# Kernel tuning notes

Hardware: AMD Instinct MI355X
Metric: run time of the kernel (lower is better)

## Reference

```python
import jax, jax.numpy as jnp
import numpy as np

N_NODES = 50000
N_EDGES = 800000
N_GRAPHS = 64
D = 90


def _kaiming_uniform(key, shape, fan_in):
    # kaiming_uniform_ with nonlinearity='relu': gain=sqrt(2), bound=gain*sqrt(3/fan_in)
    bound = np.sqrt(2.0) * np.sqrt(3.0 / fan_in)
    return jax.random.uniform(key, shape, jnp.float32, -bound, bound)


def setup_inputs() -> dict:
    key = jax.random.key(0)
    ks = jax.random.split(key, 16)
    x = jax.random.normal(ks[0], (N_NODES, D), jnp.float32)
    edge_index = jax.random.randint(ks[1], (2, N_EDGES), 0, N_NODES, jnp.int64)
    batch = jnp.sort(jax.random.randint(ks[2], (N_NODES,), 0, N_GRAPHS, jnp.int64))
    inp = {"x": x, "edge_index": edge_index, "batch": batch}
    # SAGEConv params: lin_l (neighbor path, with bias), lin_r (root path, no bias)
    for i, (kl, kr) in enumerate([(ks[3], ks[4]), (ks[5], ks[6]), (ks[7], ks[8])], start=1):
        inp[f"W{i}l"] = _kaiming_uniform(kl, (D, D), D)
        inp[f"b{i}"] = jnp.zeros((D,), jnp.float32)
        inp[f"W{i}r"] = _kaiming_uniform(kr, (D, D), D)
    inp["Wf1"] = _kaiming_uniform(ks[9], (32, D), D)
    inp["bf1"] = jnp.zeros((32,), jnp.float32)
    inp["Wf2"] = _kaiming_uniform(ks[10], (1, 32), 32)
    inp["bf2"] = jnp.zeros((1,), jnp.float32)
    return inp


def _sage_conv(x, src, dst, Wl, bl, Wr):
    # mean-aggregate neighbor messages x[src] at dst, then lin_l(agg) + lin_r(x)
    msg = x[src]                                           # [E, D] gather
    agg = jax.ops.segment_sum(msg, dst, num_segments=N_NODES)  # [N, D] scatter-add
    deg = jax.ops.segment_sum(jnp.ones((src.shape[0],), x.dtype), dst,
                              num_segments=N_NODES)
    agg = agg / jnp.maximum(deg, 1.0)[:, None]
    return agg @ Wl.T + bl + x @ Wr.T


def reference(x, edge_index, batch, W1l, b1, W1r, W2l, b2, W2r, W3l, b3, W3r,
              Wf1, bf1, Wf2, bf2):
    src, dst = edge_index[0], edge_index[1]
    h = jax.nn.relu(_sage_conv(x, src, dst, W1l, b1, W1r))
    h = jax.nn.relu(_sage_conv(h, src, dst, W2l, b2, W2r))
    h = jax.nn.relu(_sage_conv(h, src, dst, W3l, b3, W3r))
    # global_mean_pool over graph ids
    sums = jax.ops.segment_sum(h, batch, num_segments=N_GRAPHS)      # [G, D]
    cnts = jax.ops.segment_sum(jnp.ones((h.shape[0],), h.dtype), batch,
                               num_segments=N_GRAPHS)
    pooled = sums / jnp.maximum(cnts, 1.0)[:, None]
    h4 = jax.nn.relu(pooled @ Wf1.T + bf1)
    return h4 @ Wf2.T + bf2  # [G, 1]
```

## Files before the change

kernel.cpp:

```cpp
#include <hip/hip_runtime.h>
#include <hip/hip_bf16.h>

#define N_NODES 50000
#define N_PAD   50048
#define N_EDGES 800000
#define N_GRAPHS 64
#define D 90
#define HS  96
#define HSD 48
#define H8D 32
#define SC  192

#define NBUCKETS 196
#define BSHIFT 8
#define BIN_EPB 4096

typedef __attribute__((ext_vector_type(8))) short bf16x8;
typedef __attribute__((ext_vector_type(4))) float f32x4;
typedef __attribute__((ext_vector_type(2))) float f32x2;
typedef __attribute__((ext_vector_type(4))) unsigned int u32x4;

__device__ __forceinline__ float bflo(unsigned int v) { return __uint_as_float(v << 16); }
__device__ __forceinline__ float bfhi(unsigned int v) { return __uint_as_float(v & 0xffff0000u); }
__device__ __forceinline__ unsigned short bf16bits(float f) {
    __hip_bfloat16 b = __float2bfloat16(f);
    return *(unsigned short*)&b;
}
__device__ __forceinline__ unsigned int pack2bf(float lo, float hi) {
    return (unsigned int)bf16bits(lo) | ((unsigned int)bf16bits(hi) << 16);
}
__device__ __forceinline__ unsigned char f32_to_fp8(float v) {
    int pk = __builtin_amdgcn_cvt_pk_fp8_f32(v, v, 0, false);
    return (unsigned char)(pk & 0xff);
}
__device__ __forceinline__ void acc_fp8_dword(float* a, unsigned int u) {
    f32x2 lo = __builtin_amdgcn_cvt_pk_f32_fp8((int)u, false);
    f32x2 hi = __builtin_amdgcn_cvt_pk_f32_fp8((int)u, true);
    a[0] += lo.x; a[1] += lo.y; a[2] += hi.x; a[3] += hi.y;
}

__global__ void k_prep(const float* __restrict__ x, __hip_bfloat16* __restrict__ h0,
                       unsigned char* __restrict__ h8a, unsigned char* __restrict__ h8b,
                       const float* __restrict__ w1l, const float* __restrict__ w1r,
                       const float* __restrict__ w2l, const float* __restrict__ w2r,
                       const float* __restrict__ w3l, const float* __restrict__ w3r,
                       __hip_bfloat16* __restrict__ Wcat,
                       int* __restrict__ bcnt, float* __restrict__ pooled) {
    int idx = blockIdx.x * 256 + threadIdx.x;
    if (idx < N_PAD * 128) {
        int n = idx >> 7, j = idx & 127;
        float v = (n < N_NODES && j < D) ? x[n * D + j] : 0.f;
        h8a[idx] = f32_to_fp8(v);
        h8b[idx] = 0;
    }
    if (idx < N_PAD * HS) {
        int n = idx / HS, k = idx - n * HS;
        float v = (n < N_NODES && k < D) ? x[n * D + k] : 0.f;
        h0[idx] = __float2bfloat16(v);
    }
    if (idx < 3 * 96 * SC) {
        const int per = 96 * SC;
        int layer = idx / per, rem = idx - layer * per;
        int j = rem / SC, k = rem - j * SC;
        const float* wl = (layer == 0) ? w1l : (layer == 1) ? w2l : w3l;
        const float* wr = (layer == 0) ? w1r : (layer == 1) ? w2r : w3r;
        float v = 0.f;
        if (j < D) {
            if (k < 96) { if (k < D) v = wl[j * D + k]; }
            else        { int kk = k - 96; if (kk < D) v = wr[j * D + kk]; }
        }
        Wcat[idx] = __float2bfloat16(v);
    }
    if (idx < N_GRAPHS * D + N_GRAPHS) pooled[idx] = 0.f;
    if (idx < NBUCKETS) bcnt[idx] = 0;
}

__global__ void k_hist(const int* __restrict__ dst, int* __restrict__ bcnt) {
    __shared__ int h[NBUCKETS];
    int t = threadIdx.x;
    for (int i = t; i < NBUCKETS; i += 256) h[i] = 0;
    __syncthreads();
    int base = blockIdx.x * BIN_EPB;
    int lim = base + BIN_EPB; if (lim > N_EDGES) lim = N_EDGES;
    for (int e = base + t; e < lim; e += 256)
        atomicAdd(&h[dst[e] >> BSHIFT], 1);
    __syncthreads();
    for (int i = t; i < NBUCKETS; i += 256) {
        int c = h[i];
        if (c) atomicAdd(&bcnt[i], c);
    }
}

__global__ void k_bscan(const int* __restrict__ bcnt, int* __restrict__ bbase,
                        int* __restrict__ bcursor) {
    __shared__ int s[256];
    int t = threadIdx.x;
    int v = (t < NBUCKETS) ? bcnt[t] : 0;
    s[t] = v; __syncthreads();
    for (int o = 1; o < 256; o <<= 1) {
        int x = (t >= o) ? s[t - o] : 0;
        __syncthreads();
        s[t] += x;
        __syncthreads();
    }
    int excl = s[t] - v;
    if (t < NBUCKETS) { bbase[t] = excl; bcursor[t] = excl; }
    if (t == 255) bbase[NBUCKETS] = s[255];
}

__global__ __launch_bounds__(256) void k_bin(const int* __restrict__ src,
                                             const int* __restrict__ dst,
                                             int* __restrict__ bcursor,
                                             unsigned int* __restrict__ ebuf) {
    __shared__ int h[NBUCKETS];
    __shared__ int gb[NBUCKETS];
    int t = threadIdx.x;
    for (int i = t; i < NBUCKETS; i += 256) h[i] = 0;
    __syncthreads();
    int base = blockIdx.x * BIN_EPB;
    int sv[16], dv[16], rv[16];
    #pragma unroll
    for (int i = 0; i < 16; ++i) {
        int e = base + i * 256 + t;
        if (e < N_EDGES) {
            sv[i] = src[e];
            dv[i] = dst[e];
            rv[i] = atomicAdd(&h[dv[i] >> BSHIFT], 1);
        }
    }
    __syncthreads();
    for (int i = t; i < NBUCKETS; i += 256)
        gb[i] = h[i] ? atomicAdd(&bcursor[i], h[i]) : 0;
    __syncthreads();
    #pragma unroll
    for (int i = 0; i < 16; ++i) {
        int e = base + i * 256 + t;
        if (e < N_EDGES) {
            int b = dv[i] >> BSHIFT;
            ebuf[gb[b] + rv[i]] = (unsigned int)sv[i] | ((unsigned int)(dv[i] & 255) << 16);
        }
    }
}

__global__ __launch_bounds__(256) void k_fill2(const unsigned int* __restrict__ ebuf,
                                               const int* __restrict__ bbase,
                                               int* __restrict__ off,
                                               int* __restrict__ csr) {
    __shared__ int lcnt[256];
    __shared__ int excl[256];
    int t = threadIdx.x;
    int n0 = blockIdx.x << BSHIFT;
    int ebeg = bbase[blockIdx.x], eend = bbase[blockIdx.x + 1];
    lcnt[t] = 0;
    __syncthreads();
    for (int e = ebeg + t; e < eend; e += 256)
        atomicAdd(&lcnt[ebuf[e] >> 16], 1);
    __syncthreads();
    int v = lcnt[t];
    excl[t] = v; __syncthreads();
    for (int o = 1; o < 256; o <<= 1) {
        int x = (t >= o) ? excl[t - o] : 0;
        __syncthreads();
        excl[t] += x;
        __syncthreads();
    }
    excl[t] -= v;
    int n = n0 + t;
    if (n <= N_NODES) off[n] = ebeg + excl[t];
    lcnt[t] = 0;
    __syncthreads();
    for (int e = ebeg + t; e < eend; e += 256) {
        unsigned int u = ebuf[e];
        int li = u >> 16;
        int r = atomicAdd(&lcnt[li], 1);
        csr[ebeg + excl[li] + r] = (int)(u & 0xFFFFu);
    }
}

__global__ __launch_bounds__(256) void k_layer(
    const unsigned int* __restrict__ hin,
    const unsigned int* __restrict__ hin8,
    const __hip_bfloat16* __restrict__ Wcat,
    const float* __restrict__ bias,
    const int* __restrict__ off, const int* __restrict__ csr,
    __hip_bfloat16* __restrict__ hout,
    unsigned char* __restrict__ hout8)
{
    __shared__ unsigned int aggT[32][52];
    __shared__ float biasPad[96];
    int tid = threadIdx.x;
    if (tid < 96) biasPad[tid] = (tid < D) ? bias[tid] : 0.f;
    int w = tid >> 6, lane = tid & 63;

    int grp = lane >> 3, sl = lane & 7;
    int local = w * 8 + grp;
    int node = blockIdx.x * 32 + local;

    int beg = 0, end = 0;
    if (node < N_NODES) { beg = off[node]; end = off[node + 1]; }

    const u32x4* h8v = (const u32x4*)hin8;

    float a[16];
    #pragma unroll
    for (int q = 0; q < 16; ++q) a[q] = 0.f;

    int e = beg;
    for (; e + 4 <= end; e += 4) {
        u32x4 U0 = h8v[csr[e]     * 8 + sl];
        u32x4 U1 = h8v[csr[e + 1] * 8 + sl];
        u32x4 U2 = h8v[csr[e + 2] * 8 + sl];
        u32x4 U3 = h8v[csr[e + 3] * 8 + sl];
        #pragma unroll
        for (int q = 0; q < 4; ++q) acc_fp8_dword(&a[4 * q], U0[q]);
        #pragma unroll
        for (int q = 0; q < 4; ++q) acc_fp8_dword(&a[4 * q], U1[q]);
        #pragma unroll
        for (int q = 0; q < 4; ++q) acc_fp8_dword(&a[4 * q], U2[q]);
        #pragma unroll
        for (int q = 0; q < 4; ++q) acc_fp8_dword(&a[4 * q], U3[q]);
    }
    for (; e < end; ++e) {
        u32x4 U0 = h8v[csr[e] * 8 + sl];
        #pragma unroll
        for (int q = 0; q < 4; ++q) acc_fp8_dword(&a[4 * q], U0[q]);
    }

    if (sl < 6) {
        float inv = 1.0f / fmaxf((float)(end - beg), 1.0f);
        #pragma unroll
        for (int q = 0; q < 8; ++q) {
            int c0 = 16 * sl + 2 * q;
            float lo = (c0     < D) ? a[2 * q]     * inv : 0.f;
            float hi = (c0 + 1 < D) ? a[2 * q + 1] * inv : 0.f;
            aggT[local][8 * sl + q] = pack2bf(lo, hi);
        }
    }
    __syncthreads();

    int w2 = w & 1, half = w >> 1;
    int mrow = lane & 15, kg = lane >> 4;
    int r0 = blockIdx.x * 32 + w2 * 16;
    int lrow = w2 * 16 + mrow;
    const short* Wp = (const short*)Wcat;
    const short* Hs = (const short*)hin;

    f32x4 acc[3];
    #pragma unroll
    for (int t = 0; t < 3; ++t) {
        int j = (half * 3 + t) * 16 + mrow;
        float b = biasPad[j];
        acc[t] = (f32x4){b, b, b, b};
    }

    #pragma unroll
    for (int ks = 0; ks < 6; ++ks) {
        bf16x8 afr;
        if (ks < 3) afr = *(const bf16x8*)&aggT[lrow][ks * 16 + kg * 4];
        else        afr = *(const bf16x8*)&Hs[(r0 + mrow) * HS + (ks - 3) * 32 + kg * 8];
        #pragma unroll
        for (int t = 0; t < 3; ++t) {
            int j = (half * 3 + t) * 16 + mrow;
            bf16x8 bfr = *(const bf16x8*)&Wp[j * SC + ks * 32 + kg * 8];
            acc[t] = __builtin_amdgcn_mfma_f32_16x16x32_bf16(afr, bfr, acc[t], 0, 0, 0);
        }
    }

    int orow = r0 + kg * 4;
    #pragma unroll
    for (int t = 0; t < 3; ++t) {
        int j = (half * 3 + t) * 16 + mrow;
        #pragma unroll
        for (int v = 0; v < 4; ++v) {
            float val = (j < D) ? fmaxf(acc[t][v], 0.f) : 0.f;
            hout[(orow + v) * HS + j] = __float2bfloat16(val);
            hout8[(orow + v) * 128 + j] = f32_to_fp8(val);
        }
    }
}

#define POOL_WAVES 4096
__global__ void k_pool(const unsigned int* __restrict__ h, const int* __restrict__ batch,
                       float* __restrict__ pooled, float* __restrict__ cntg) {
    int wid  = (blockIdx.x * blockDim.x + threadIdx.x) >> 6;
    int lane = threadIdx.x & 63;
    const int per = (N_NODES + POOL_WAVES - 1) / POOL_WAVES;
    int beg = wid * per;
    int end = beg + per; if (end > N_NODES) end = N_NODES;
    if (beg >= end) return;
    int cur = batch[beg];
    float a0 = 0.f, a1 = 0.f, c = 0.f;
    for (int n = beg; n < end; ++n) {
        int g = batch[n];
        if (g != cur) {
            if (lane < 45) {
                atomicAdd(&pooled[cur * D + 2 * lane], a0);
                atomicAdd(&pooled[cur * D + 2 * lane + 1], a1);
            }
            if (lane == 0) atomicAdd(&cntg[cur], c);
            a0 = a1 = c = 0.f;
            cur = g;
        }
        if (lane < 45) {
            unsigned int v = h[n * HSD + lane];
            a0 += bflo(v);
            a1 += bfhi(v);
        }
        c += 1.f;
    }
    if (lane < 45) {
        atomicAdd(&pooled[cur * D + 2 * lane], a0);
        atomicAdd(&pooled[cur * D + 2 * lane + 1], a1);
    }
    if (lane == 0) atomicAdd(&cntg[cur], c);
}

__global__ void k_mlp(const float* __restrict__ pooled, const float* __restrict__ cntg,
                      const float* __restrict__ Wf1, const float* __restrict__ bf1,
                      const float* __restrict__ Wf2, const float* __restrict__ bf2,
                      float* __restrict__ outp) {
    __shared__ float P[N_GRAPHS][92];
    __shared__ float H4[N_GRAPHS][32];
    int tid = threadIdx.x;
    for (int idx = tid; idx < N_GRAPHS * D; idx += 256) {
        int g = idx / D, d = idx - g * D;
        P[g][d] = pooled[idx] / fmaxf(cntg[g], 1.0f);
    }
    __syncthreads();
    for (int idx = tid; idx < N_GRAPHS * 32; idx += 256) {
        int g = idx >> 5, c = idx & 31;
        float acc = bf1[c];
        for (int d = 0; d < D; ++d) acc += P[g][d] * Wf1[c * D + d];
        H4[g][c] = fmaxf(acc, 0.f);
    }
    __syncthreads();
    if (tid < N_GRAPHS) {
        float acc = bf2[0];
        #pragma unroll
        for (int c = 0; c < 32; ++c) acc += H4[tid][c] * Wf2[c];
        outp[tid] = acc;
    }
}

extern "C" void kernel_launch(void* const* d_in, const int* in_sizes, int n_in,
                              void* d_out, int out_size, void* d_ws, size_t ws_size,
                              hipStream_t stream) {
    const float* x    = (const float*)d_in[0];
    const int*   ei   = (const int*)d_in[1];
    const int*   batch= (const int*)d_in[2];
    const float* W1l  = (const float*)d_in[3];
    const float* b1   = (const float*)d_in[4];
    const float* W1r  = (const float*)d_in[5];
    const float* W2l  = (const float*)d_in[6];
    const float* b2   = (const float*)d_in[7];
    const float* W2r  = (const float*)d_in[8];
    const float* W3l  = (const float*)d_in[9];
    const float* b3   = (const float*)d_in[10];
    const float* W3r  = (const float*)d_in[11];
    const float* Wf1  = (const float*)d_in[12];
    const float* bf1  = (const float*)d_in[13];
    const float* Wf2  = (const float*)d_in[14];
    const float* bf2  = (const float*)d_in[15];
    const int* srcI = ei;
    const int* dstI = ei + N_EDGES;

    char* base = (char*)d_ws;
    size_t o = 0;
    auto alloc = [&](size_t bytes) -> void* {
        void* p = base + o;
        o = (o + bytes + 255) & ~(size_t)255;
        return p;
    };
    int*   bcnt    = (int*)alloc((size_t)NBUCKETS * 4);
    int*   bbase   = (int*)alloc((size_t)(NBUCKETS + 1) * 4);
    int*   bcursor = (int*)alloc((size_t)NBUCKETS * 4);
    int*   off     = (int*)alloc((size_t)(N_NODES + 1) * 4);
    unsigned int* ebuf = (unsigned int*)alloc((size_t)N_EDGES * 4);
    int*   csr     = (int*)alloc((size_t)N_EDGES * 4);
    __hip_bfloat16* hA = (__hip_bfloat16*)alloc((size_t)N_PAD * HS * 2);
    __hip_bfloat16* hB = (__hip_bfloat16*)alloc((size_t)N_PAD * HS * 2);
    unsigned char* h8A = (unsigned char*)alloc((size_t)N_PAD * 128);
    unsigned char* h8B = (unsigned char*)alloc((size_t)N_PAD * 128);
    __hip_bfloat16* Wcat = (__hip_bfloat16*)alloc((size_t)3 * 96 * SC * 2);
    float* pooled = (float*)alloc((size_t)(N_GRAPHS * D + N_GRAPHS) * 4);
    float* cntg   = pooled + N_GRAPHS * D;

    k_prep<<<(N_PAD * 128 + 255) / 256, 256, 0, stream>>>(
        x, hA, h8A, h8B, W1l, W1r, W2l, W2r, W3l, W3r, Wcat, bcnt, pooled);

    const int EB = (N_EDGES + BIN_EPB - 1) / BIN_EPB;
    k_hist<<<EB, 256, 0, stream>>>(dstI, bcnt);
    k_bscan<<<1, 256, 0, stream>>>(bcnt, bbase, bcursor);
    k_bin<<<EB, 256, 0, stream>>>(srcI, dstI, bcursor, ebuf);
    k_fill2<<<NBUCKETS, 256, 0, stream>>>(ebuf, bbase, off, csr);

    const int LAYER_BLOCKS = N_PAD / 32;

    unsigned int* hAu  = (unsigned int*)hA;
    unsigned int* hBu  = (unsigned int*)hB;
    unsigned int* h8Au = (unsigned int*)h8A;
    unsigned int* h8Bu = (unsigned int*)h8B;

    k_layer<<<LAYER_BLOCKS, 256, 0, stream>>>(hAu, h8Au, Wcat,            b1, off, csr, hB, h8B);
    k_layer<<<LAYER_BLOCKS, 256, 0, stream>>>(hBu, h8Bu, Wcat +  96 * SC, b2, off, csr, hA, h8A);
    k_layer<<<LAYER_BLOCKS, 256, 0, stream>>>(hAu, h8Au, Wcat + 192 * SC, b3, off, csr, hB, h8B);

    k_pool<<<POOL_WAVES / 4, 256, 0, stream>>>(hBu, batch, pooled, cntg);
    k_mlp<<<1, 256, 0, stream>>>(pooled, cntg, Wf1, bf1, Wf2, bf2, (float*)d_out);
}
```

Measured before the change: 200.6 us.

## Fuse edge histogram into prep kernel, vectorize prep stores, unroll gather by eight

Merges the dst-bucket histogram into the prep kernel as extra blocks that write per-block partial counts, with the scan summing those partials instead of relying on global atomics. This removes one launch and the zeroing of the counters. Prep now writes packed 32-bit words (two bf16 or four fp8 values) per thread, so it needs far fewer threads and issues wider stores. The layer gather loop adds an 8-edge unrolled stage to keep more loads in flight, which costs extra registers.

```diff
diff --git a/kernel.cpp b/kernel.cpp
--- a/kernel.cpp
+++ b/kernel.cpp
@@ -8,12 +8,12 @@
 #define D 90
 #define HS  96
 #define HSD 48
-#define H8D 32
 #define SC  192
 
 #define NBUCKETS 196
 #define BSHIFT 8
 #define BIN_EPB 4096
+#define PREP_BLOCKS 9384
 
 typedef __attribute__((ext_vector_type(8))) short bf16x8;
 typedef __attribute__((ext_vector_type(4))) float f32x4;
@@ -39,24 +39,48 @@
     a[0] += lo.x; a[1] += lo.y; a[2] += hi.x; a[3] += hi.y;
 }
 
-__global__ void k_prep(const float* __restrict__ x, __hip_bfloat16* __restrict__ h0,
-                       unsigned char* __restrict__ h8a, unsigned char* __restrict__ h8b,
-                       const float* __restrict__ w1l, const float* __restrict__ w1r,
-                       const float* __restrict__ w2l, const float* __restrict__ w2r,
-                       const float* __restrict__ w3l, const float* __restrict__ w3r,
-                       __hip_bfloat16* __restrict__ Wcat,
-                       int* __restrict__ bcnt, float* __restrict__ pooled) {
+__global__ __launch_bounds__(256) void k_prep(
+    const float* __restrict__ x, unsigned int* __restrict__ h0u,
+    unsigned int* __restrict__ h8a, unsigned int* __restrict__ h8b,
+    const float* __restrict__ w1l, const float* __restrict__ w1r,
+    const float* __restrict__ w2l, const float* __restrict__ w2r,
+    const float* __restrict__ w3l, const float* __restrict__ w3r,
+    __hip_bfloat16* __restrict__ Wcat, float* __restrict__ pooled,
+    const int* __restrict__ dst, int* __restrict__ hpart) {
+    if (blockIdx.x >= PREP_BLOCKS) {
+        __shared__ int h[NBUCKETS];
+        int t = threadIdx.x;
+        for (int i = t; i < NBUCKETS; i += 256) h[i] = 0;
+        __syncthreads();
+        int hb = blockIdx.x - PREP_BLOCKS;
+        int base = hb * BIN_EPB;
+        int lim = base + BIN_EPB; if (lim > N_EDGES) lim = N_EDGES;
+        for (int e = base + t; e < lim; e += 256)
+            atomicAdd(&h[dst[e] >> BSHIFT], 1);
+        __syncthreads();
+        for (int i = t; i < NBUCKETS; i += 256)
+            hpart[hb * NBUCKETS + i] = h[i];
+        return;
+    }
     int idx = blockIdx.x * 256 + threadIdx.x;
-    if (idx < N_PAD * 128) {
-        int n = idx >> 7, j = idx & 127;
-        float v = (n < N_NODES && j < D) ? x[n * D + j] : 0.f;
-        h8a[idx] = f32_to_fp8(v);
-        h8b[idx] = 0;
-    }
-    if (idx < N_PAD * HS) {
-        int n = idx / HS, k = idx - n * HS;
-        float v = (n < N_NODES && k < D) ? x[n * D + k] : 0.f;
-        h0[idx] = __float2bfloat16(v);
+    {
+        int n = idx / 48, kd = idx - n * 48;
+        int c0 = 2 * kd;
+        float v0 = (n < N_NODES && c0     < D) ? x[n * D + c0]     : 0.f;
+        float v1 = (n < N_NODES && c0 + 1 < D) ? x[n * D + c0 + 1] : 0.f;
+        h0u[idx] = pack2bf(v0, v1);
+    }
+    if (idx < N_PAD * 32) {
+        int n = idx >> 5, jd = idx & 31;
+        int c0 = 4 * jd;
+        float v0 = (n < N_NODES && c0     < D) ? x[n * D + c0]     : 0.f;
+        float v1 = (n < N_NODES && c0 + 1 < D) ? x[n * D + c0 + 1] : 0.f;
+        float v2 = (n < N_NODES && c0 + 2 < D) ? x[n * D + c0 + 2] : 0.f;
+        float v3 = (n < N_NODES && c0 + 3 < D) ? x[n * D + c0 + 3] : 0.f;
+        int t0 = __builtin_amdgcn_cvt_pk_fp8_f32(v0, v1, 0, false);
+        t0 = __builtin_amdgcn_cvt_pk_fp8_f32(v2, v3, t0, true);
+        h8a[idx] = (unsigned int)t0;
+        h8b[idx] = 0u;
     }
     if (idx < 3 * 96 * SC) {
         const int per = 96 * SC;
@@ -72,30 +96,16 @@
         Wcat[idx] = __float2bfloat16(v);
     }
     if (idx < N_GRAPHS * D + N_GRAPHS) pooled[idx] = 0.f;
-    if (idx < NBUCKETS) bcnt[idx] = 0;
-}
-
-__global__ void k_hist(const int* __restrict__ dst, int* __restrict__ bcnt) {
-    __shared__ int h[NBUCKETS];
-    int t = threadIdx.x;
-    for (int i = t; i < NBUCKETS; i += 256) h[i] = 0;
-    __syncthreads();
-    int base = blockIdx.x * BIN_EPB;
-    int lim = base + BIN_EPB; if (lim > N_EDGES) lim = N_EDGES;
-    for (int e = base + t; e < lim; e += 256)
-        atomicAdd(&h[dst[e] >> BSHIFT], 1);
-    __syncthreads();
-    for (int i = t; i < NBUCKETS; i += 256) {
-        int c = h[i];
-        if (c) atomicAdd(&bcnt[i], c);
-    }
-}
-
-__global__ void k_bscan(const int* __restrict__ bcnt, int* __restrict__ bbase,
+}
+
+__global__ void k_bscan(const int* __restrict__ hpart, int* __restrict__ bbase,
                         int* __restrict__ bcursor) {
     __shared__ int s[256];
     int t = threadIdx.x;
-    int v = (t < NBUCKETS) ? bcnt[t] : 0;
+    int v = 0;
+    if (t < NBUCKETS) {
+        for (int b = 0; b < 196; ++b) v += hpart[b * NBUCKETS + t];
+    }
     s[t] = v; __syncthreads();
     for (int o = 1; o < 256; o <<= 1) {
         int x = (t >= o) ? s[t - o] : 0;
@@ -206,19 +216,25 @@
     for (int q = 0; q < 16; ++q) a[q] = 0.f;
 
     int e = beg;
+    for (; e + 8 <= end; e += 8) {
+        u32x4 U[8];
+        #pragma unroll
+        for (int r = 0; r < 8; ++r) U[r] = h8v[csr[e + r] * 8 + sl];
+        #pragma unroll
+        for (int r = 0; r < 8; ++r) {
+            #pragma unroll
+            for (int q = 0; q < 4; ++q) acc_fp8_dword(&a[4 * q], U[r][q]);
+        }
+    }
     for (; e + 4 <= end; e += 4) {
-        u32x4 U0 = h8v[csr[e]     * 8 + sl];
-        u32x4 U1 = h8v[csr[e + 1] * 8 + sl];
-        u32x4 U2 = h8v[csr[e + 2] * 8 + sl];
-        u32x4 U3 = h8v[csr[e + 3] * 8 + sl];
-        #pragma unroll
-        for (int q = 0; q < 4; ++q) acc_fp8_dword(&a[4 * q], U0[q]);
-        #pragma unroll
-        for (int q = 0; q < 4; ++q) acc_fp8_dword(&a[4 * q], U1[q]);
-        #pragma unroll
-        for (int q = 0; q < 4; ++q) acc_fp8_dword(&a[4 * q], U2[q]);
-        #pragma unroll
-        for (int q = 0; q < 4; ++q) acc_fp8_dword(&a[4 * q], U3[q]);
+        u32x4 U[4];
+        #pragma unroll
+        for (int r = 0; r < 4; ++r) U[r] = h8v[csr[e + r] * 8 + sl];
+        #pragma unroll
+        for (int r = 0; r < 4; ++r) {
+            #pragma unroll
+            for (int q = 0; q < 4; ++q) acc_fp8_dword(&a[4 * q], U[r][q]);
+        }
     }
     for (; e < end; ++e) {
         u32x4 U0 = h8v[csr[e] * 8 + sl];
@@ -371,7 +387,7 @@
         o = (o + bytes + 255) & ~(size_t)255;
         return p;
     };
-    int*   bcnt    = (int*)alloc((size_t)NBUCKETS * 4);
+    int*   hpart   = (int*)alloc((size_t)196 * NBUCKETS * 4);
     int*   bbase   = (int*)alloc((size_t)(NBUCKETS + 1) * 4);
     int*   bcursor = (int*)alloc((size_t)NBUCKETS * 4);
     int*   off     = (int*)alloc((size_t)(N_NODES + 1) * 4);
@@ -385,22 +401,21 @@
     float* pooled = (float*)alloc((size_t)(N_GRAPHS * D + N_GRAPHS) * 4);
     float* cntg   = pooled + N_GRAPHS * D;
 
-    k_prep<<<(N_PAD * 128 + 255) / 256, 256, 0, stream>>>(
-        x, hA, h8A, h8B, W1l, W1r, W2l, W2r, W3l, W3r, Wcat, bcnt, pooled);
-
-    const int EB = (N_EDGES + BIN_EPB - 1) / BIN_EPB;
-    k_hist<<<EB, 256, 0, stream>>>(dstI, bcnt);
-    k_bscan<<<1, 256, 0, stream>>>(bcnt, bbase, bcursor);
-    k_bin<<<EB, 256, 0, stream>>>(srcI, dstI, bcursor, ebuf);
-    k_fill2<<<NBUCKETS, 256, 0, stream>>>(ebuf, bbase, off, csr);
-
-    const int LAYER_BLOCKS = N_PAD / 32;
-
     unsigned int* hAu  = (unsigned int*)hA;
     unsigned int* hBu  = (unsigned int*)hB;
     unsigned int* h8Au = (unsigned int*)h8A;
     unsigned int* h8Bu = (unsigned int*)h8B;
 
+    const int EB = (N_EDGES + BIN_EPB - 1) / BIN_EPB;
+    k_prep<<<PREP_BLOCKS + EB, 256, 0, stream>>>(
+        x, hAu, h8Au, h8Bu, W1l, W1r, W2l, W2r, W3l, W3r, Wcat, pooled, dstI, hpart);
+
+    k_bscan<<<1, 256, 0, stream>>>(hpart, bbase, bcursor);
+    k_bin<<<EB, 256, 0, stream>>>(srcI, dstI, bcursor, ebuf);
+    k_fill2<<<NBUCKETS, 256, 0, stream>>>(ebuf, bbase, off, csr);
+
+    const int LAYER_BLOCKS = N_PAD / 32;
+
     k_layer<<<LAYER_BLOCKS, 256, 0, stream>>>(hAu, h8Au, Wcat,            b1, off, csr, hB, h8B);
     k_layer<<<LAYER_BLOCKS, 256, 0, stream>>>(hBu, h8Bu, Wcat +  96 * SC, b2, off, csr, hA, h8A);
     k_layer<<<LAYER_BLOCKS, 256, 0, stream>>>(hAu, h8Au, Wcat + 192 * SC, b3, off, csr, hB, h8B);
```

Measured after the change: 207.6 us. 3.5% more time.
